# Kernel optimization log

Measured on AMD Instinct MI355X. Metric: run time of the kernel, lower is better.

Reference implementation:

```python
import jax, jax.numpy as jnp
import numpy as np

DIM = 128
SCALE = (DIM // 8) ** -0.5  # head_dim**-0.5 with default num_heads=8 (heads never actually split)


def _attention(x, fm, qw, kw, vw, pw, pb):
    # x, fm: [B, C, H, W]
    B, C, H, W = x.shape
    xt = x.reshape(B, C, H * W).transpose(0, 2, 1)   # [B, N, C]
    ft = fm.reshape(B, C, H * W).transpose(0, 2, 1)  # [B, N, C]
    q = jnp.einsum('bnc,dc->bnd', xt, qw)
    k = jnp.einsum('bnc,dc->bnd', ft, kw)
    v = jnp.einsum('bnc,dc->bnd', xt, vw)
    attn = jax.nn.softmax(jnp.einsum('bnd,bmd->bnm', q, k) * SCALE, axis=-1)
    o = jnp.einsum('bnm,bmd->bnd', attn, v)
    o = jnp.einsum('bnd,ed->bne', o, pw) + pb
    return o.transpose(0, 2, 1).reshape(B, C, H, W)


def setup_inputs() -> dict:
    key = jax.random.key(0)
    ks = jax.random.split(key, 16)
    B, C, H, W = 1, DIM, 96, 96
    s = 0.02
    inp = {
        'x': jax.random.normal(ks[0], (B, C, H, W), jnp.float32),
        'featuremap': jax.random.normal(ks[1], (B, C, H, W), jnp.float32),
        'hm': jax.random.uniform(ks[2], (B, 1, H, W), jnp.float32),
        'obj_qw': jax.random.normal(ks[3], (C, C), jnp.float32) * s,
        'obj_kw': jax.random.normal(ks[4], (C, C), jnp.float32) * s,
        'obj_vw': jax.random.normal(ks[5], (C, C), jnp.float32) * s,
        'obj_pw': jax.random.normal(ks[6], (C, C), jnp.float32) * s,
        'obj_pb': jnp.zeros((C,), jnp.float32),
        'bg_qw': jax.random.normal(ks[7], (C, C), jnp.float32) * s,
        'bg_kw': jax.random.normal(ks[8], (C, C), jnp.float32) * s,
        'bg_vw': jax.random.normal(ks[9], (C, C), jnp.float32) * s,
        'bg_pw': jax.random.normal(ks[10], (C, C), jnp.float32) * s,
        'bg_pb': jnp.zeros((C,), jnp.float32),
        'conv_w': jax.random.normal(ks[11], (C, C, 3, 3), jnp.float32) * s,
        'conv_b': jnp.zeros((C,), jnp.float32),
    }
    return inp


def reference(x, featuremap, hm, obj_qw, obj_kw, obj_vw, obj_pw, obj_pb,
              bg_qw, bg_kw, bg_vw, bg_pw, bg_pb, conv_w, conv_b):
    obj_mask = jnp.where(hm > 0.3, 1.0, 0.01)
    bg_mask = jnp.where(hm <= 0.3, 1.0, 0.01)
    obj_att = _attention(x * obj_mask, featuremap * obj_mask,
                         obj_qw, obj_kw, obj_vw, obj_pw, obj_pb)
    bg_att = _attention(x * bg_mask, featuremap * bg_mask,
                        bg_qw, bg_kw, bg_vw, bg_pw, bg_pb)
    am = obj_att + bg_att
    out = jax.lax.conv_general_dilated(
        am, conv_w, window_strides=(1, 1), padding='SAME',
        dimension_numbers=('NCHW', 'OIHW', 'NCHW'))
    return out + conv_b[None, :, None, None]
```

## Files before the change

### kernel.cpp

```cpp
#include <hip/hip_runtime.h>


typedef unsigned short u16;
typedef short bf16x8 __attribute__((ext_vector_type(8)));
typedef float f32x4 __attribute__((ext_vector_type(4)));

#define MFMA(a, b, c) __builtin_amdgcn_mfma_f32_16x16x32_bf16((a), (b), (c), 0, 0, 0)

#define NN 9216
#define CC 128
#define SPLIT 8
#define FITERS 36

__device__ __forceinline__ u16 f2b(float f) {
  union { float f; unsigned int u; } v; v.f = f;
  unsigned int u = v.u + 0x7fffu + ((v.u >> 16) & 1u);
  return (u16)(u >> 16);
}

__device__ __forceinline__ unsigned int f2b2(float lo, float hi) {
  return (unsigned int)f2b(lo) | ((unsigned int)f2b(hi) << 16);
}

__device__ __forceinline__ unsigned int pkhi(float a, float b) {
  return __builtin_amdgcn_perm(__float_as_uint(b), __float_as_uint(a), 0x07060302u);
}

__device__ __forceinline__ bf16x8 ldb(const u16* p) { return *(const bf16x8*)p; }

__global__ void k_prep(const float* __restrict__ x, const float* __restrict__ fm,
                       const float* qw0, const float* kw0, const float* vw0,
                       const float* pw0, const float* qw1, const float* kw1,
                       const float* vw1, const float* pw1,
                       const float* __restrict__ cw,
                       u16* __restrict__ xt, u16* __restrict__ fmt,
                       u16* __restrict__ wall, u16* __restrict__ wp) {
  int bid = blockIdx.x, tid = threadIdx.x;
  if (bid < 2304) {
    __shared__ float tile[32][33];
    int z = bid / 1152, b2 = bid % 1152;
    const float* src = z ? fm : x;
    u16* dst = z ? fmt : xt;
    int n0 = (b2 % 288) * 32, c0 = (b2 / 288) * 32;
    int tx = tid & 31, ty = tid >> 5;
#pragma unroll
    for (int i = 0; i < 4; i++)
      tile[ty + i * 8][tx] = src[(c0 + ty + i * 8) * NN + n0 + tx];
    __syncthreads();
#pragma unroll
    for (int i = 0; i < 4; i++)
      dst[(n0 + ty + i * 8) * CC + c0 + tx] = f2b(tile[tx][ty + i * 8]);
  } else if (bid < 2816) {
    const float* arr[8] = {qw0, kw0, vw0, pw0, qw1, kw1, vw1, pw1};
    int b2 = bid - 2304;
    int a = b2 >> 6;
    int i = (b2 & 63) * 256 + tid;
    wall[a * 16384 + i] = f2b(arr[a][i]);
  } else {
    int i = (bid - 2816) * 256 + tid;
    int khkw = i >> 14; int rem = i & 16383; int o = rem >> 7; int ii = rem & 127;
    wp[i] = f2b(cw[(o * 128 + ii) * 9 + khkw]);
  }
}

__global__ __launch_bounds__(256) void k_qkv(
    const u16* __restrict__ xt, const u16* __restrict__ fmt, const float* __restrict__ hm,
    const u16* __restrict__ wall, u16* __restrict__ Q, u16* __restrict__ K,
    u16* __restrict__ Vt) {
  __shared__ __align__(16) u16 sst[8192];
  int tid = threadIdx.x;
  int wid = tid >> 6, lane = tid & 63;
  int quad = lane >> 4, c = lane & 15;
  int nb64 = blockIdx.x * 64;
  int nb = nb64 + wid * 16;
  int arr = blockIdx.y;
  int attn = arr / 3, kind = arr % 3;
  const u16* A = (kind == 1) ? fmt : xt;
  const u16* W = wall + (attn * 4 + kind) * 16384;

  bf16x8 wf[2][4];
#pragma unroll
  for (int k4 = 0; k4 < 4; k4++)
    wf[0][k4] = ldb(W + c * CC + k4 * 32 + quad * 8);

  if (kind < 2) {
    bf16x8 af[4];
#pragma unroll
    for (int k4 = 0; k4 < 4; k4++)
      af[k4] = ldb(A + (nb + c) * CC + k4 * 32 + quad * 8);
    float msk[4];
#pragma unroll
    for (int r = 0; r < 4; r++) {
      bool obj = hm[nb + quad * 4 + r] > 0.3f;
      float mv = (attn == 0) ? (obj ? 1.f : 0.01f) : (obj ? 0.01f : 1.f);
      msk[r] = (kind == 0) ? mv * 0.3606737602222409f : mv;
    }
    u16* tw = sst + wid * 2048;
#pragma unroll
    for (int dt = 0; dt < 8; dt++) {
      int cur = dt & 1;
      if (dt < 7) {
#pragma unroll
        for (int k4 = 0; k4 < 4; k4++)
          wf[cur ^ 1][k4] = ldb(W + ((dt + 1) * 16 + c) * CC + k4 * 32 + quad * 8);
      }
      f32x4 acc = {0.f, 0.f, 0.f, 0.f};
#pragma unroll
      for (int k4 = 0; k4 < 4; k4++)
        acc = MFMA(af[k4], wf[cur][k4], acc);
#pragma unroll
      for (int r = 0; r < 4; r++)
        tw[(quad * 4 + r) * 128 + dt * 16 + c] = f2b(acc[r] * msk[r]);
    }
    u16* out = (kind == 0 ? Q : K) + attn * NN * CC + nb * CC;
#pragma unroll
    for (int i = 0; i < 4; i++) {
      uint4 v = *(const uint4*)((const char*)tw + i * 1024 + lane * 16);
      *(uint4*)((char*)out + i * 1024 + lane * 16) = v;
    }
  } else {
    bf16x8 bfr[4];
#pragma unroll
    for (int k4 = 0; k4 < 4; k4++)
      bfr[k4] = ldb(A + (nb + c) * CC + k4 * 32 + quad * 8);
    bool obj = hm[nb + c] > 0.3f;
    float mv = (attn == 0) ? (obj ? 1.f : 0.01f) : (obj ? 0.01f : 1.f);
#pragma unroll
    for (int dt = 0; dt < 8; dt++) {
      int cur = dt & 1;
      if (dt < 7) {
#pragma unroll
        for (int k4 = 0; k4 < 4; k4++)
          wf[cur ^ 1][k4] = ldb(W + ((dt + 1) * 16 + c) * CC + k4 * 32 + quad * 8);
      }
      f32x4 acc = {0.f, 0.f, 0.f, 0.f};
#pragma unroll
      for (int k4 = 0; k4 < 4; k4++)
        acc = MFMA(wf[cur][k4], bfr[k4], acc);
#pragma unroll
      for (int r = 0; r < 4; r++)
        sst[(dt * 16 + quad * 4 + r) * 64 + wid * 16 + c] = f2b(acc[r] * mv);
    }
    __syncthreads();
    char* vt0 = (char*)(Vt + attn * CC * NN) + nb64 * 2;
#pragma unroll
    for (int i = 0; i < 4; i++) {
      int idx = wid * 4 + i;
      int drow = idx * 8 + (lane >> 3);
      int ch = lane & 7;
      uint4 v = *(const uint4*)((const char*)sst + drow * 128 + ch * 16);
      *(uint4*)(vt0 + (long)drow * (NN * 2) + ch * 16) = v;
    }
  }
}

__global__ __launch_bounds__(256, 3) void k_flash(
    const u16* __restrict__ Q, const u16* __restrict__ K, const u16* __restrict__ Vt,
    u16* __restrict__ U, float* __restrict__ L) {
  __shared__ __align__(16) char lds[47104];
  int tid = threadIdx.x;
  int wid = tid >> 6, lane = tid & 63;
  int quad = lane >> 4, c = lane & 15;
  int b = blockIdx.x;
  int qg = b >> 4; int combo = b & 15;
  int attn = combo >> 3; int ks = combo & 7;
  int nb = qg * 128 + wid * 32;
  const u16* q = Q + attn * NN * CC;
  const u16* kg = K + attn * NN * CC;
  const u16* vg = Vt + attn * CC * NN;
  int kb0 = ks * 1152;

  int krow = tid >> 4, kch = tid & 15;
  const u16* gkp0 = kg + (kb0 + krow) * CC + kch * 8;
  const u16* gkp1 = gkp0 + 16 * CC;
  int lk0 = krow * 256 + ((kch ^ (krow & 7)) * 16);
  int lk1 = lk0 + 4096;
  int vrow = tid >> 2, vqd = tid & 3;
  const u16* gvp0 = vg + vrow * NN + kb0 + vqd * 8;
  const u16* gvp1 = gvp0 + 64 * NN;
  int lv0 = vrow * 80 + vqd * 16, lv1 = lv0 + 64 * 80;

  bf16x8 qf[2][4];
#pragma unroll
  for (int qt = 0; qt < 2; qt++)
#pragma unroll
    for (int k4 = 0; k4 < 4; k4++)
      qf[qt][k4] = ldb(q + (nb + qt * 16 + c) * CC + k4 * 32 + quad * 8);

  const bf16x8 ONES = {(short)0x3F80, (short)0x3F80, (short)0x3F80, (short)0x3F80,
                       (short)0x3F80, (short)0x3F80, (short)0x3F80, (short)0x3F80};

  f32x4 O[2][8];
  f32x4 lacc[2];
#pragma unroll
  for (int qt = 0; qt < 2; qt++) {
#pragma unroll
    for (int dt = 0; dt < 8; dt++) O[qt][dt] = (f32x4){0.f, 0.f, 0.f, 0.f};
    lacc[qt] = (f32x4){0.f, 0.f, 0.f, 0.f};
  }

  char* Pw = lds + 36864 + wid * 2560;

  uint4 gk0 = *(const uint4*)gkp0, gk1 = *(const uint4*)gkp1;
  uint4 gv0 = *(const uint4*)gvp0, gv1 = *(const uint4*)gvp1;

  for (int it = 0; it < FITERS; it++) {
    char* kb_lds = lds + ((it & 1) ? 8192 : 0);
    char* vb_lds = lds + 16384 + ((it & 1) ? 10240 : 0);
    *(uint4*)(kb_lds + lk0) = gk0;
    *(uint4*)(kb_lds + lk1) = gk1;
    *(uint4*)(vb_lds + lv0) = gv0;
    *(uint4*)(vb_lds + lv1) = gv1;
    if (it + 1 < FITERS) {
      gkp0 += 32 * CC; gkp1 += 32 * CC; gvp0 += 32; gvp1 += 32;
      gk0 = *(const uint4*)gkp0; gk1 = *(const uint4*)gkp1;
      gv0 = *(const uint4*)gvp0; gv1 = *(const uint4*)gvp1;
    }
    __syncthreads();

#pragma unroll
    for (int kt = 0; kt < 2; kt++) {
      bf16x8 kf[4];
#pragma unroll
      for (int k4 = 0; k4 < 4; k4++)
        kf[k4] = *(const bf16x8*)(kb_lds + (kt * 16 + c) * 256 +
                                  (((k4 * 4 + quad) ^ (c & 7)) * 16));
#pragma unroll
      for (int qt = 0; qt < 2; qt++) {
        f32x4 s = {0.f, 0.f, 0.f, 0.f};
#pragma unroll
        for (int k4 = 0; k4 < 4; k4++) s = MFMA(kf[k4], qf[qt][k4], s);
        uint2 d;
        d.x = pkhi(__builtin_amdgcn_exp2f(s[0]), __builtin_amdgcn_exp2f(s[1]));
        d.y = pkhi(__builtin_amdgcn_exp2f(s[2]), __builtin_amdgcn_exp2f(s[3]));
        *(uint2*)(Pw + (qt * 16 + c) * 80 + kt * 32 + quad * 8) = d;
      }
    }

    bf16x8 pf[2];
#pragma unroll
    for (int qt = 0; qt < 2; qt++) {
      pf[qt] = *(const bf16x8*)(Pw + (qt * 16 + c) * 80 + quad * 16);
      lacc[qt] = MFMA(pf[qt], ONES, lacc[qt]);
    }
#pragma unroll
    for (int dt = 0; dt < 8; dt++) {
      bf16x8 vf = *(const bf16x8*)(vb_lds + (dt * 16 + c) * 80 + quad * 16);
#pragma unroll
      for (int qt = 0; qt < 2; qt++) O[qt][dt] = MFMA(pf[qt], vf, O[qt][dt]);
    }
  }

  int p = attn * SPLIT + ks;
  u16* up = U + (long)(p * NN + nb) * CC;
#pragma unroll
  for (int qt = 0; qt < 2; qt++)
#pragma unroll
    for (int dt = 0; dt < 8; dt++)
#pragma unroll
      for (int r = 0; r < 4; r++)
        up[(qt * 16 + quad * 4 + r) * CC + dt * 16 + c] = f2b(O[qt][dt][r]);
  if (c == 0) {
#pragma unroll
    for (int qt = 0; qt < 2; qt++)
#pragma unroll
      for (int r = 0; r < 4; r++)
        L[p * NN + nb + qt * 16 + quad * 4 + r] = lacc[qt][r];
  }
}

__global__ __launch_bounds__(256) void k_pm(const u16* __restrict__ U,
                                            const float* __restrict__ L,
                                            const u16* __restrict__ wall,
                                            const float* __restrict__ pb0,
                                            const float* __restrict__ pb1,
                                            u16* __restrict__ amt) {
  __shared__ __align__(16) char omt[8704];
  __shared__ float linv[32];
  int tid = threadIdx.x;
  int nb = blockIdx.x * 16;

  {
    if (tid < 32) {
      int a = tid >> 4, r = tid & 15;
      float l = 0.f;
#pragma unroll
      for (int s = 0; s < SPLIT; s++) l += L[(a * SPLIT + s) * NN + nb + r];
      linv[tid] = 1.f / l;
    }
    int a = tid >> 7, rr = (tid >> 3) & 15, dg = tid & 7;
    uint4 ua[SPLIT], ub[SPLIT];
#pragma unroll
    for (int s = 0; s < SPLIT; s++) {
      const u16* src = U + (long)((a * SPLIT + s) * NN + nb + rr) * CC + dg * 16;
      ua[s] = *(const uint4*)src;
      ub[s] = *(const uint4*)(src + 8);
    }
    float acc[16];
#pragma unroll
    for (int j = 0; j < 16; j++) acc[j] = 0.f;
#pragma unroll
    for (int s = 0; s < SPLIT; s++) {
      const unsigned int* w0 = (const unsigned int*)&ua[s];
      const unsigned int* w1 = (const unsigned int*)&ub[s];
#pragma unroll
      for (int j = 0; j < 4; j++) {
        acc[j * 2 + 0] += __uint_as_float(w0[j] << 16);
        acc[j * 2 + 1] += __uint_as_float(w0[j] & 0xffff0000u);
        acc[8 + j * 2 + 0] += __uint_as_float(w1[j] << 16);
        acc[8 + j * 2 + 1] += __uint_as_float(w1[j] & 0xffff0000u);
      }
    }
    __syncthreads();
    float inv = linv[a * 16 + rr];
    unsigned int pk[8];
#pragma unroll
    for (int j = 0; j < 8; j++)
      pk[j] = f2b2(acc[j * 2] * inv, acc[j * 2 + 1] * inv);
    uint4* dst = (uint4*)(omt + (a * 16 + rr) * 272 + dg * 32);
    dst[0] = *(uint4*)&pk[0];
    dst[1] = *(uint4*)&pk[4];
  }
  __syncthreads();

  int wid = tid >> 6, lane = tid & 63;
  int quad = lane >> 4, c = lane & 15;
  bf16x8 af[2][4];
#pragma unroll
  for (int a = 0; a < 2; a++)
#pragma unroll
    for (int k4 = 0; k4 < 4; k4++)
      af[a][k4] = *(const bf16x8*)(omt + (a * 16 + c) * 272 + k4 * 64 + quad * 16);
  const u16* wpo = wall + 3 * 16384;
  const u16* wpb = wall + 7 * 16384;
  __syncthreads();
  u16* pmt = (u16*)omt;
#pragma unroll
  for (int eh = 0; eh < 2; eh++) {
    int et = wid * 2 + eh;
    f32x4 acc = {0.f, 0.f, 0.f, 0.f};
#pragma unroll
    for (int k4 = 0; k4 < 4; k4++)
      acc = MFMA(af[0][k4], ldb(wpo + (et * 16 + c) * CC + k4 * 32 + quad * 8), acc);
#pragma unroll
    for (int k4 = 0; k4 < 4; k4++)
      acc = MFMA(af[1][k4], ldb(wpb + (et * 16 + c) * CC + k4 * 32 + quad * 8), acc);
    float bias = pb0[et * 16 + c] + pb1[et * 16 + c];
#pragma unroll
    for (int r = 0; r < 4; r++)
      pmt[(quad * 4 + r) * 128 + et * 16 + c] = f2b(acc[r] + bias);
  }
  __syncthreads();
  uint4 v = *(const uint4*)((const char*)pmt + wid * 1024 + lane * 16);
  *(uint4*)((char*)(amt + nb * CC) + wid * 1024 + lane * 16) = v;
}

__global__ __launch_bounds__(256) void k_conv(const u16* __restrict__ amt,
                                              const u16* __restrict__ wp,
                                              const float* __restrict__ cb,
                                              float* __restrict__ out) {
  int wid = threadIdx.x >> 6, lane = threadIdx.x & 63;
  int quad = lane >> 4, c = lane & 15;
  int p = blockIdx.x * 16 + c;
  int h = p / 96, w = p % 96;
  f32x4 acc0 = {0.f, 0.f, 0.f, 0.f};
  f32x4 acc1 = {0.f, 0.f, 0.f, 0.f};
  const bf16x8 zv = {0, 0, 0, 0, 0, 0, 0, 0};
  int ot0 = wid * 2, ot1 = wid * 2 + 1;

  bf16x8 bv[2][4], wa[2][4], wb[2][4];

#define LOAD_TAP(BUF, T)                                                      \
  {                                                                           \
    int kh = (T) / 3, kw = (T) % 3;                                           \
    int hh = h + kh - 1, ww = w + kw - 1;                                     \
    bool valid = (hh >= 0) && (hh < 96) && (ww >= 0) && (ww < 96);            \
    int sp = hh * 96 + ww;                                                    \
    const u16* wbase = wp + (T) * 16384;                                      \
    _Pragma("unroll") for (int k4 = 0; k4 < 4; k4++) {                        \
      bv[BUF][k4] = valid ? ldb(amt + sp * CC + k4 * 32 + quad * 8) : zv;     \
      wa[BUF][k4] = ldb(wbase + (ot0 * 16 + c) * CC + k4 * 32 + quad * 8);    \
      wb[BUF][k4] = ldb(wbase + (ot1 * 16 + c) * CC + k4 * 32 + quad * 8);    \
    }                                                                         \
  }

  LOAD_TAP(0, 0)
#pragma unroll
  for (int t = 0; t < 9; t++) {
    int cur = t & 1;
    if (t < 8) LOAD_TAP(cur ^ 1, t + 1)
#pragma unroll
    for (int k4 = 0; k4 < 4; k4++) {
      acc0 = MFMA(wa[cur][k4], bv[cur][k4], acc0);
      acc1 = MFMA(wb[cur][k4], bv[cur][k4], acc1);
    }
  }
#undef LOAD_TAP

#pragma unroll
  for (int r = 0; r < 4; r++) {
    int o0 = ot0 * 16 + quad * 4 + r;
    int o1 = ot1 * 16 + quad * 4 + r;
    out[o0 * NN + p] = acc0[r] + cb[o0];
    out[o1 * NN + p] = acc1[r] + cb[o1];
  }
}

extern "C" void kernel_launch(void* const* d_in, const int* in_sizes, int n_in,
                              void* d_out, int out_size, void* d_ws, size_t ws_size,
                              hipStream_t stream) {
  (void)in_sizes; (void)n_in; (void)out_size; (void)ws_size;
  const float* x   = (const float*)d_in[0];
  const float* fm  = (const float*)d_in[1];
  const float* hm  = (const float*)d_in[2];
  const float* qw0 = (const float*)d_in[3];
  const float* kw0 = (const float*)d_in[4];
  const float* vw0 = (const float*)d_in[5];
  const float* pw0 = (const float*)d_in[6];
  const float* pb0 = (const float*)d_in[7];
  const float* qw1 = (const float*)d_in[8];
  const float* kw1 = (const float*)d_in[9];
  const float* vw1 = (const float*)d_in[10];
  const float* pw1 = (const float*)d_in[11];
  const float* pb1 = (const float*)d_in[12];
  const float* cw  = (const float*)d_in[13];
  const float* cb  = (const float*)d_in[14];
  float* out = (float*)d_out;
  char* ws = (char*)d_ws;

  u16*   XT   = (u16*)(ws + 0);
  u16*   FMT  = (u16*)(ws + 2359296);
  u16*   WALL = (u16*)(ws + 4718592);
  u16*   WCV  = (u16*)(ws + 4980736);
  u16*   QQ   = (u16*)(ws + 5275648);
  u16*   KK   = (u16*)(ws + 9994240);
  u16*   VT   = (u16*)(ws + 14712832);
  u16*   UU   = (u16*)(ws + 19431424);
  float* LL   = (float*)(ws + 57180160);
  u16*   AMT  = KK;

  k_prep<<<3392, 256, 0, stream>>>(x, fm, qw0, kw0, vw0, pw0, qw1, kw1, vw1, pw1,
                                   cw, XT, FMT, WALL, WCV);
  k_qkv<<<dim3(144, 6), 256, 0, stream>>>(XT, FMT, hm, WALL, QQ, KK, VT);
  k_flash<<<1152, 256, 0, stream>>>(QQ, KK, VT, UU, LL);
  k_pm<<<576, 256, 0, stream>>>(UU, LL, WALL, pb0, pb1, AMT);
  k_conv<<<576, 256, 0, stream>>>(AMT, WCV, cb, out);
}
```

Before: 249.3 us.

## Load K tiles via direct global-to-LDS DMA and stage conv halo in LDS

In the flash kernel, K tiles now go straight into LDS through global_load_lds, with the XOR swizzle moved to the global source address, and the prefetch for the next tile is issued after the barrier. This removes the register round trip for K. The flash kernel's launch bound drops from 3 to 2 blocks per SM, which gives the compiler more registers but may lower occupancy. The conv kernel now stages an 18x3 pixel halo tile of the activation in LDS once per block, so the 9 taps read it from LDS instead of reloading from global memory with per-tap bounds checks.

```diff
diff --git a/kernel.cpp b/kernel.cpp
--- a/kernel.cpp
+++ b/kernel.cpp
@@ -27,6 +27,12 @@
 }
 
 __device__ __forceinline__ bf16x8 ldb(const u16* p) { return *(const bf16x8*)p; }
+
+__device__ __forceinline__ void ldsdma16(const void* g, void* l) {
+  __builtin_amdgcn_global_load_lds(
+      (const __attribute__((address_space(1))) unsigned int*)g,
+      (__attribute__((address_space(3))) unsigned int*)l, 16, 0, 0);
+}
 
 __global__ void k_prep(const float* __restrict__ x, const float* __restrict__ fm,
                        const float* qw0, const float* kw0, const float* vw0,
@@ -154,7 +160,7 @@
   }
 }
 
-__global__ __launch_bounds__(256, 3) void k_flash(
+__global__ __launch_bounds__(256, 2) void k_flash(
     const u16* __restrict__ Q, const u16* __restrict__ K, const u16* __restrict__ Vt,
     u16* __restrict__ U, float* __restrict__ L) {
   __shared__ __align__(16) char lds[47104];
@@ -170,11 +176,10 @@
   const u16* vg = Vt + attn * CC * NN;
   int kb0 = ks * 1152;
 
-  int krow = tid >> 4, kch = tid & 15;
-  const u16* gkp0 = kg + (kb0 + krow) * CC + kch * 8;
+  int srow = tid >> 4;
+  int chn = (tid & 15) ^ (srow & 7);
+  const u16* gkp0 = kg + (kb0 + srow) * CC + chn * 8;
   const u16* gkp1 = gkp0 + 16 * CC;
-  int lk0 = krow * 256 + ((kch ^ (krow & 7)) * 16);
-  int lk1 = lk0 + 4096;
   int vrow = tid >> 2, vqd = tid & 3;
   const u16* gvp0 = vg + vrow * NN + kb0 + vqd * 8;
   const u16* gvp1 = gvp0 + 64 * NN;
@@ -201,22 +206,24 @@
 
   char* Pw = lds + 36864 + wid * 2560;
 
-  uint4 gk0 = *(const uint4*)gkp0, gk1 = *(const uint4*)gkp1;
+  ldsdma16(gkp0, lds + wid * 1024);
+  ldsdma16(gkp1, lds + 4096 + wid * 1024);
   uint4 gv0 = *(const uint4*)gvp0, gv1 = *(const uint4*)gvp1;
 
   for (int it = 0; it < FITERS; it++) {
     char* kb_lds = lds + ((it & 1) ? 8192 : 0);
     char* vb_lds = lds + 16384 + ((it & 1) ? 10240 : 0);
-    *(uint4*)(kb_lds + lk0) = gk0;
-    *(uint4*)(kb_lds + lk1) = gk1;
     *(uint4*)(vb_lds + lv0) = gv0;
     *(uint4*)(vb_lds + lv1) = gv1;
+    __syncthreads();
     if (it + 1 < FITERS) {
-      gkp0 += 32 * CC; gkp1 += 32 * CC; gvp0 += 32; gvp1 += 32;
-      gk0 = *(const uint4*)gkp0; gk1 = *(const uint4*)gkp1;
+      char* kn = lds + (((it + 1) & 1) ? 8192 : 0);
+      gkp0 += 32 * CC; gkp1 += 32 * CC;
+      ldsdma16(gkp0, kn + wid * 1024);
+      ldsdma16(gkp1, kn + 4096 + wid * 1024);
+      gvp0 += 32; gvp1 += 32;
       gv0 = *(const uint4*)gvp0; gv1 = *(const uint4*)gvp1;
     }
-    __syncthreads();
 
 #pragma unroll
     for (int kt = 0; kt < 2; kt++) {
@@ -359,43 +366,54 @@
                                               const u16* __restrict__ wp,
                                               const float* __restrict__ cb,
                                               float* __restrict__ out) {
-  int wid = threadIdx.x >> 6, lane = threadIdx.x & 63;
+  __shared__ __align__(16) char halo[54 * 272];
+  int tid = threadIdx.x;
+  int wid = tid >> 6, lane = tid & 63;
   int quad = lane >> 4, c = lane & 15;
-  int p = blockIdx.x * 16 + c;
-  int h = p / 96, w = p % 96;
+  int p0 = blockIdx.x * 16;
+  int h = p0 / 96, w0 = p0 % 96;
+
+  for (int t = tid; t < 54 * 16; t += 256) {
+    int hp = t >> 4, ch16 = t & 15;
+    int hr = hp / 18, hc = hp % 18;
+    int hh = h + hr - 1, ww = w0 + hc - 1;
+    uint4 v = {0u, 0u, 0u, 0u};
+    if (hh >= 0 && hh < 96 && ww >= 0 && ww < 96)
+      v = *(const uint4*)(amt + (hh * 96 + ww) * CC + ch16 * 8);
+    *(uint4*)(halo + hp * 272 + ch16 * 16) = v;
+  }
+  __syncthreads();
+
+  int p = p0 + c;
   f32x4 acc0 = {0.f, 0.f, 0.f, 0.f};
   f32x4 acc1 = {0.f, 0.f, 0.f, 0.f};
-  const bf16x8 zv = {0, 0, 0, 0, 0, 0, 0, 0};
   int ot0 = wid * 2, ot1 = wid * 2 + 1;
 
-  bf16x8 bv[2][4], wa[2][4], wb[2][4];
-
-#define LOAD_TAP(BUF, T)                                                      \
+  bf16x8 wa[2][4], wb[2][4];
+#define LOAD_W(BUF, T)                                                        \
   {                                                                           \
-    int kh = (T) / 3, kw = (T) % 3;                                           \
-    int hh = h + kh - 1, ww = w + kw - 1;                                     \
-    bool valid = (hh >= 0) && (hh < 96) && (ww >= 0) && (ww < 96);            \
-    int sp = hh * 96 + ww;                                                    \
     const u16* wbase = wp + (T) * 16384;                                      \
     _Pragma("unroll") for (int k4 = 0; k4 < 4; k4++) {                        \
-      bv[BUF][k4] = valid ? ldb(amt + sp * CC + k4 * 32 + quad * 8) : zv;     \
       wa[BUF][k4] = ldb(wbase + (ot0 * 16 + c) * CC + k4 * 32 + quad * 8);    \
       wb[BUF][k4] = ldb(wbase + (ot1 * 16 + c) * CC + k4 * 32 + quad * 8);    \
     }                                                                         \
   }
 
-  LOAD_TAP(0, 0)
+  LOAD_W(0, 0)
 #pragma unroll
   for (int t = 0; t < 9; t++) {
     int cur = t & 1;
-    if (t < 8) LOAD_TAP(cur ^ 1, t + 1)
+    if (t < 8) LOAD_W(cur ^ 1, t + 1)
+    int kh = t / 3, kw = t % 3;
+    const char* hrow = halo + (kh * 18 + kw + c) * 272;
 #pragma unroll
     for (int k4 = 0; k4 < 4; k4++) {
-      acc0 = MFMA(wa[cur][k4], bv[cur][k4], acc0);
-      acc1 = MFMA(wb[cur][k4], bv[cur][k4], acc1);
-    }
-  }
-#undef LOAD_TAP
+      bf16x8 bv = *(const bf16x8*)(hrow + k4 * 64 + quad * 16);
+      acc0 = MFMA(wa[cur][k4], bv, acc0);
+      acc1 = MFMA(wb[cur][k4], bv, acc1);
+    }
+  }
+#undef LOAD_W
 
 #pragma unroll
   for (int r = 0; r < 4; r++) {
```

Result: faster. 241.7 us (-3.0%).
